# Kernel tuning notes

Measured on AMD Instinct MI355X. Metric: run time of the kernel, lower is better.

Reference implementation:

```python
import jax, jax.numpy as jnp
import numpy as np

B, S, D, H = 2, 2048, 1024, 16
DK = D // H


def setup_inputs() -> dict:
    key = jax.random.key(0)
    ks = jax.random.split(key, 8)
    s = 1.0 / np.sqrt(D)
    return {
        "query": jax.random.normal(ks[0], (B, S, D), jnp.float32),
        "key": jax.random.normal(ks[1], (B, S, D), jnp.float32),
        "value": jax.random.normal(ks[2], (B, S, D), jnp.float32),
        "mask": jnp.ones((B, S), jnp.int32),
        "w_q": jax.random.normal(ks[3], (D, D), jnp.float32) * s,
        "w_k": jax.random.normal(ks[4], (D, D), jnp.float32) * s,
        "w_v": jax.random.normal(ks[5], (D, D), jnp.float32) * s,
        "w_o": jax.random.normal(ks[6], (D, D), jnp.float32) * s,
        "b_o": jnp.zeros((D,), jnp.float32),
    }


def reference(query, key, value, mask, w_q, w_k, w_v, w_o, b_o):
    scale = np.sqrt(DK).astype(np.float32)
    # Linear layers: torch stores weight as [out, in], y = x @ W.T
    Q = (query @ w_q.T).reshape(B, S, H, DK).transpose(0, 2, 1, 3)  # [B,H,S,DK]
    K = (key @ w_k.T).reshape(B, S, H, DK).transpose(0, 2, 1, 3)
    V = (value @ w_v.T).reshape(B, S, H, DK).transpose(0, 2, 1, 3)
    scores = jnp.einsum("bhqd,bhkd->bhqk", Q, K) / scale  # [B,H,S,S]
    m = mask[:, None, None, :]  # [B,1,1,S]
    scores = jnp.where(m == 0, jnp.float32(-1e9), scores)
    attn = jax.nn.softmax(scores, axis=-1)  # dropout in eval mode = identity
    ctx = jnp.einsum("bhqk,bhkd->bhqd", attn, V)
    ctx = ctx.transpose(0, 2, 1, 3).reshape(B, S, D)
    out = ctx @ w_o.T + b_o
    return out, attn
```

## Files before the change

### kernel.cpp

```cpp
#include <hip/hip_runtime.h>
#include <hip/hip_bf16.h>
#include <math.h>

#define B 2
#define S 2048
#define D 1024
#define H 16
#define DK 64

typedef __attribute__((ext_vector_type(8))) short bf8;
typedef __attribute__((ext_vector_type(8))) unsigned short u16x8;
typedef __attribute__((ext_vector_type(4))) unsigned short u16x4;
typedef __attribute__((ext_vector_type(4))) float f32x4;
typedef unsigned short ush;

__device__ __forceinline__ float bf2f(ush u) {
    union { unsigned int i; float f; } v; v.i = ((unsigned int)u) << 16; return v.f;
}
__device__ __forceinline__ ush f2bf_rne(float x) {
    __hip_bfloat16 h = __float2bfloat16(x);
    union { __hip_bfloat16 h; ush u; } v; v.h = h; return v.u;
}
__device__ __forceinline__ ush f2bf_trunc(float x) {
    union { float f; unsigned int i; } v; v.f = x; return (ush)(v.i >> 16);
}

__device__ __forceinline__ void gl16(const void* g, void* l) {
    __builtin_amdgcn_global_load_lds(
        (const __attribute__((address_space(1))) void*)g,
        (__attribute__((address_space(3))) void*)l, 16, 0, 0);
}

#define FENCE()    asm volatile("" ::: "memory")
#define WAIT_VM(N) asm volatile("s_waitcnt vmcnt(" #N ")" ::: "memory")
#define BARRAW()   __builtin_amdgcn_s_barrier()

__global__ __launch_bounds__(256) void conv_tri_k(
    const float* __restrict__ A, ush* __restrict__ Ah, ush* __restrict__ Al, int nbA,
    const float* __restrict__ Bsrc, ush* __restrict__ Bh, ush* __restrict__ Bl, int nbB,
    const float* __restrict__ C, ush* __restrict__ Ch)
{
    const int bx = blockIdx.x;
    const float* src; ush* oh; ush* ol; size_t t;
    if (bx < nbA)            { src = A;    oh = Ah; ol = Al;      t = (size_t)bx * 256 + threadIdx.x; }
    else if (bx < nbA + nbB) { src = Bsrc; oh = Bh; ol = Bl;      t = (size_t)(bx - nbA) * 256 + threadIdx.x; }
    else                     { src = C;    oh = Ch; ol = nullptr; t = (size_t)(bx - nbA - nbB) * 256 + threadIdx.x; }

    const float4* s4 = (const float4*)src + t * 2;
    float4 a = s4[0], c = s4[1];
    float v[8] = {a.x, a.y, a.z, a.w, c.x, c.y, c.z, c.w};
    u16x8 hi;
#pragma unroll
    for (int j = 0; j < 8; ++j) hi[j] = f2bf_trunc(v[j]);
    *(u16x8*)&oh[t * 8] = hi;
    if (ol) {
        u16x8 lo;
#pragma unroll
        for (int j = 0; j < 8; ++j) lo[j] = f2bf_rne(v[j] - bf2f(hi[j]));
        *(u16x8*)&ol[t * 8] = lo;
    }
}

template<bool SPLIT, int EPI>
__global__ __launch_bounds__(256) void gemm_bf2(
    const ush* __restrict__ Xh, const ush* __restrict__ Xl,
    const ush* __restrict__ Wh, const ush* __restrict__ Wl,
    const float* __restrict__ bias, void* __restrict__ Y0v, void* __restrict__ Y1v)
{
    const int tid  = threadIdx.x;
    const int lane = tid & 63;
    const int w    = tid >> 6;
    const int wn   = w >> 1, wm = w & 1;
    const int m0   = blockIdx.x * 64;
    const int n0   = blockIdx.y * 128;

    __shared__ __align__(16) ush Xs[2][128 * 64];
    __shared__ __align__(16) ush Ws[2][64 * 64];

    f32x4 acc[4][2];
#pragma unroll
    for (int s = 0; s < 4; ++s)
#pragma unroll
        for (int t = 0; t < 2; ++t) acc[s][t] = (f32x4){0.f, 0.f, 0.f, 0.f};

    const int kg = (lane >> 4) * 8;
    const int rb = lane >> 3;
    const int jd = lane & 7;
    const int kSteps = SPLIT ? 32 : 16;

    auto stage = [&](ush* Xd, ush* Wd, int ks) {
#pragma unroll
        for (int i = 0; i < 4; ++i) {
            int rd = i * 32 + w * 8 + rb;
            int jo = jd ^ (rd & 7);
            const ush* src;
            if (SPLIT)
                src = (jo < 4) ? Xh + (size_t)(n0 + rd) * 1024 + ks * 32 + jo * 8
                               : Xl + (size_t)(n0 + rd) * 1024 + ks * 32 + (jo - 4) * 8;
            else
                src = Xh + (size_t)(n0 + rd) * 1024 + ks * 64 + jo * 8;
            gl16(src, &Xd[(i * 32 + w * 8) * 64]);
        }
#pragma unroll
        for (int i = 0; i < 2; ++i) {
            int rd = i * 32 + w * 8 + rb;
            int jo = jd ^ (rd & 7);
            const ush* src;
            if (SPLIT)
                src = (jo < 4) ? Wh + (size_t)(m0 + rd) * 1024 + ks * 32 + jo * 8
                               : Wl + (size_t)(m0 + rd) * 1024 + ks * 32 + (jo - 4) * 8;
            else
                src = Wh + (size_t)(m0 + rd) * 1024 + ks * 64 + jo * 8;
            gl16(src, &Wd[(i * 32 + w * 8) * 64]);
        }
    };

    auto step = [&](const ush* Xsrc, const ush* Wsrc) {
        bf8 a0[4], a1[4], b0[2], b1[2];
#pragma unroll
        for (int s = 0; s < 4; ++s) {
            int r = wn * 64 + s * 16 + (lane & 15);
            a0[s] = *(const bf8*)&Xsrc[r * 64 + (kg ^ ((r & 7) << 3))];
            a1[s] = *(const bf8*)&Xsrc[r * 64 + ((32 + kg) ^ ((r & 7) << 3))];
        }
#pragma unroll
        for (int t = 0; t < 2; ++t) {
            int r = wm * 32 + t * 16 + (lane & 15);
            b0[t] = *(const bf8*)&Wsrc[r * 64 + (kg ^ ((r & 7) << 3))];
            b1[t] = *(const bf8*)&Wsrc[r * 64 + ((32 + kg) ^ ((r & 7) << 3))];
        }
#pragma unroll
        for (int s = 0; s < 4; ++s)
#pragma unroll
            for (int t = 0; t < 2; ++t) {
                acc[s][t] = __builtin_amdgcn_mfma_f32_16x16x32_bf16(a0[s], b0[t], acc[s][t], 0, 0, 0);
                if (SPLIT) {
                    acc[s][t] = __builtin_amdgcn_mfma_f32_16x16x32_bf16(a0[s], b1[t], acc[s][t], 0, 0, 0);
                    acc[s][t] = __builtin_amdgcn_mfma_f32_16x16x32_bf16(a1[s], b0[t], acc[s][t], 0, 0, 0);
                } else {
                    acc[s][t] = __builtin_amdgcn_mfma_f32_16x16x32_bf16(a1[s], b1[t], acc[s][t], 0, 0, 0);
                }
            }
    };

    stage(Xs[0], Ws[0], 0);
    FENCE();
    WAIT_VM(0); BARRAW(); FENCE();
    for (int k2 = 0; k2 < kSteps / 2; ++k2) {
        stage(Xs[1], Ws[1], 2 * k2 + 1);
        FENCE();
        step(Xs[0], Ws[0]);
        WAIT_VM(0); BARRAW(); FENCE();
        if (2 * k2 + 2 < kSteps) { stage(Xs[0], Ws[0], 2 * k2 + 2); FENCE(); }
        step(Xs[1], Ws[1]);
        WAIT_VM(0); BARRAW(); FENCE();
    }

#pragma unroll
    for (int s = 0; s < 4; ++s)
#pragma unroll
        for (int t = 0; t < 2; ++t) {
            const int nb = n0 + wn * 64 + 16 * s + 4 * (lane >> 4);
            const int m  = m0 + wm * 32 + 16 * t + (lane & 15);
            if (EPI == 1) {
                ush* Yh = (ush*)Y0v;
                ush* Yl = (ush*)Y1v;
#pragma unroll
                for (int r = 0; r < 4; ++r) {
                    float v = acc[s][t][r];
                    ush hi = f2bf_trunc(v);
                    Yh[(size_t)(nb + r) * 1024 + m] = hi;
                    Yl[(size_t)(nb + r) * 1024 + m] = f2bf_rne(v - bf2f(hi));
                }
            } else {
                ush* Vt = (ush*)Y0v;
                u16x4 pk;
#pragma unroll
                for (int r = 0; r < 4; ++r) pk[r] = f2bf_rne(acc[s][t][r]);
                size_t addr = ((size_t)(nb >> 11) * 1024 + m) * 2048 + (nb & 2047);
                *(u16x4*)&Vt[addr] = pk;
            }
        }
}

__global__ __launch_bounds__(256) void gemm_out(
    const ush* __restrict__ Xb, const float* __restrict__ W,
    const float* __restrict__ bias, float* __restrict__ Y)
{
    const int tid  = threadIdx.x;
    const int lane = tid & 63;
    const int w    = tid >> 6;
    const int wn   = w >> 1, wm = w & 1;
    const int m0   = blockIdx.x * 64;
    const int n0   = blockIdx.y * 128;

    __shared__ __align__(16) ush Xs[128 * 64];
    __shared__ __align__(16) ush Ws[64 * 64];

    f32x4 acc[4][2];
#pragma unroll
    for (int s = 0; s < 4; ++s)
#pragma unroll
        for (int t = 0; t < 2; ++t) acc[s][t] = (f32x4){0.f, 0.f, 0.f, 0.f};

    const int kg = (lane >> 4) * 8;

    for (int k0 = 0; k0 < 1024; k0 += 32) {
        __syncthreads();
#pragma unroll
        for (int i = 0; i < 2; ++i) {
            int cid = i * 256 + tid;
            int r = cid >> 2, c = (cid & 3) * 8;
            u16x8 v = *(const u16x8*)&Xb[(size_t)(n0 + r) * 1024 + k0 + c];
            *(u16x8*)&Xs[r * 64 + (c ^ ((r & 7) << 3))] = v;
        }
#pragma unroll
        for (int i = 0; i < 2; ++i) {
            int cid = i * 256 + tid;
            int r = cid >> 3, c = (cid & 7) * 4;
            float4 v = *(const float4*)&W[(size_t)(m0 + r) * 1024 + k0 + c];
            float vv[4] = {v.x, v.y, v.z, v.w};
            u16x4 hi;
#pragma unroll
            for (int j = 0; j < 4; ++j) hi[j] = f2bf_trunc(vv[j]);
            *(u16x4*)&Ws[r * 64 + (c ^ ((r & 7) << 3))] = hi;
        }
        __syncthreads();

        bf8 ah[4], bh[2];
#pragma unroll
        for (int s = 0; s < 4; ++s) {
            int r = wn * 64 + s * 16 + (lane & 15);
            ah[s] = *(const bf8*)&Xs[r * 64 + (kg ^ ((r & 7) << 3))];
        }
#pragma unroll
        for (int t = 0; t < 2; ++t) {
            int r = wm * 32 + t * 16 + (lane & 15);
            bh[t] = *(const bf8*)&Ws[r * 64 + (kg ^ ((r & 7) << 3))];
        }
#pragma unroll
        for (int s = 0; s < 4; ++s)
#pragma unroll
            for (int t = 0; t < 2; ++t)
                acc[s][t] = __builtin_amdgcn_mfma_f32_16x16x32_bf16(ah[s], bh[t], acc[s][t], 0, 0, 0);
    }

#pragma unroll
    for (int s = 0; s < 4; ++s)
#pragma unroll
        for (int t = 0; t < 2; ++t) {
            const int nb = n0 + wn * 64 + 16 * s + 4 * (lane >> 4);
            const int m  = m0 + wm * 32 + 16 * t + (lane & 15);
            const float bb = bias[m];
#pragma unroll
            for (int r = 0; r < 4; ++r)
                Y[(size_t)(nb + r) * 1024 + m] = acc[s][t][r] + bb;
        }
}

__global__ __launch_bounds__(512) void attn_mfma4(
    const ush* __restrict__ Qh, const ush* __restrict__ Ql,
    const ush* __restrict__ Kh, const ush* __restrict__ Kl,
    const ush* __restrict__ Vt, const int* __restrict__ maskg,
    float* __restrict__ attn, ush* __restrict__ ctx)
{
    const int tid  = threadIdx.x;
    const int lane = tid & 63;
    const int w    = tid >> 6;
    const int lid  = blockIdx.x + (blockIdx.y << 4) + (blockIdx.z << 8);
    const int swz  = ((lid & 7) << 6) | (lid >> 3);
    const int qt = swz & 15, h = (swz >> 4) & 15, b = swz >> 8;
    const int q0 = qt * 128;

    __shared__ __align__(16) ush KhsD[3][4096];
    __shared__ __align__(16) ush KlsD[2][4096];
    __shared__ __align__(16) ush VtsD[2][4096];
    __shared__ __align__(16) ush Pus[8][1024];
    __shared__ float biasS[2048];

    const int kg = (lane >> 4) * 8;
    const int q  = lane & 15;
    const int qrow = q0 + w * 16 + q;
    const int rb = lane >> 3;
    const int jd = lane & 7;

    const ush* KhT = Kh + (size_t)(b * S) * 1024 + h * DK;
    const ush* KlT = Kl + (size_t)(b * S) * 1024 + h * DK;
    const ush* VtT = Vt + (size_t)(b * 1024 + h * DK) * 2048;

    {
        const int t4 = tid * 4;
        int4 mv = *(const int4*)&maskg[b * S + t4];
        biasS[t4 + 0] = mv.x ? 0.f : -1e9f;
        biasS[t4 + 1] = mv.y ? 0.f : -1e9f;
        biasS[t4 + 2] = mv.z ? 0.f : -1e9f;
        biasS[t4 + 3] = mv.w ? 0.f : -1e9f;
    }

    bf8 qh[2], ql[2];
    {
        const ush* p1 = Qh + (size_t)(b * S + qrow) * D + h * DK + kg;
        qh[0] = *(const bf8*)p1; qh[1] = *(const bf8*)(p1 + 32);
        const ush* p2 = Ql + (size_t)(b * S + qrow) * D + h * DK + kg;
        ql[0] = *(const bf8*)p2; ql[1] = *(const bf8*)(p2 + 32);
    }

    const int rd = w * 8 + rb;
    const int jo = jd ^ (rd & 7);

    auto stKh = [&](int bufi, int k0) {
        gl16(KhT + (size_t)(k0 + rd) * 1024 + jo * 8, &KhsD[bufi][(w * 8) * 64]);
    };
    auto stKl = [&](int bufi, int k0) {
        gl16(KlT + (size_t)(k0 + rd) * 1024 + jo * 8, &KlsD[bufi][(w * 8) * 64]);
    };
    auto stVt = [&](int bufi, int k0) {
        gl16(VtT + (size_t)rd * 2048 + k0 + jo * 8, &VtsD[bufi][(w * 8) * 64]);
    };

    const float scale = 0.125f;
    float mrow = -1e30f, lrow = 0.f;

    auto computeA = [&](const ush* Khs_, int k0) {
        f32x4 sacc[4];
#pragma unroll
        for (int st = 0; st < 4; ++st) sacc[st] = (f32x4){0.f, 0.f, 0.f, 0.f};
#pragma unroll
        for (int st = 0; st < 4; ++st) {
            int r = st * 16 + q;
#pragma unroll
            for (int dh = 0; dh < 2; ++dh) {
                bf8 kf = *(const bf8*)&Khs_[r * 64 + ((dh * 32 + kg) ^ ((r & 7) << 3))];
                sacc[st] = __builtin_amdgcn_mfma_f32_16x16x32_bf16(kf, qh[dh], sacc[st], 0, 0, 0);
            }
        }
        f32x4 bias_r[4];
#pragma unroll
        for (int st = 0; st < 4; ++st)
            bias_r[st] = *(const f32x4*)&biasS[k0 + st * 16 + (lane >> 4) * 4];
        float tmax = -1e30f;
#pragma unroll
        for (int st = 0; st < 4; ++st)
#pragma unroll
            for (int rr = 0; rr < 4; ++rr)
                tmax = fmaxf(tmax, sacc[st][rr] * scale + bias_r[st][rr]);
        tmax = fmaxf(tmax, __shfl_xor(tmax, 16));
        tmax = fmaxf(tmax, __shfl_xor(tmax, 32));
        const float nm = fmaxf(mrow, tmax);
        float ts = 0.f;
#pragma unroll
        for (int st = 0; st < 4; ++st)
#pragma unroll
            for (int rr = 0; rr < 4; ++rr)
                ts += __expf(sacc[st][rr] * scale + bias_r[st][rr] - nm);
        ts += __shfl_xor(ts, 16);
        ts += __shfl_xor(ts, 32);
        lrow = lrow * __expf(mrow - nm) + ts;
        mrow = nm;
    };

    stKh(0, 0); stKh(1, 64);
    __syncthreads();
    {
        int cur = 0, nxt = 2;
        for (int kt = 0; kt < 32; ++kt) {
            if (kt + 2 < 32) stKh(nxt, (kt + 2) * 64);
            FENCE();
            computeA(&KhsD[cur][0], kt * 64);
            if (kt < 30) { WAIT_VM(1); } else { WAIT_VM(0); }
            BARRAW(); FENCE();
            cur = (cur == 2) ? 0 : cur + 1;
            nxt = (nxt == 2) ? 0 : nxt + 1;
        }
    }
    const float inv_l = 1.f / lrow;

    f32x4 cacc[4];
#pragma unroll
    for (int dt = 0; dt < 4; ++dt) cacc[dt] = (f32x4){0.f, 0.f, 0.f, 0.f};
    float* attn_bh = attn + (size_t)(b * H + h) * S * S;

    auto computeB = [&](int bsel, int k0) {
        const ush* Khs_ = &KhsD[bsel][0];
        const ush* Kls_ = &KlsD[bsel][0];
        const ush* Vts_ = &VtsD[bsel][0];
        f32x4 sacc[4];
#pragma unroll
        for (int st = 0; st < 4; ++st) sacc[st] = (f32x4){0.f, 0.f, 0.f, 0.f};
#pragma unroll
        for (int st = 0; st < 4; ++st) {
            int r = st * 16 + q;
#pragma unroll
            for (int dh = 0; dh < 2; ++dh) {
                bf8 kf = *(const bf8*)&Khs_[r * 64 + ((dh * 32 + kg) ^ ((r & 7) << 3))];
                bf8 lf = *(const bf8*)&Kls_[r * 64 + ((dh * 32 + kg) ^ ((r & 7) << 3))];
                sacc[st] = __builtin_amdgcn_mfma_f32_16x16x32_bf16(kf, qh[dh], sacc[st], 0, 0, 0);
                sacc[st] = __builtin_amdgcn_mfma_f32_16x16x32_bf16(kf, ql[dh], sacc[st], 0, 0, 0);
                sacc[st] = __builtin_amdgcn_mfma_f32_16x16x32_bf16(lf, qh[dh], sacc[st], 0, 0, 0);
            }
        }
#pragma unroll
        for (int st = 0; st < 4; ++st) {
            f32x4 bias_r = *(const f32x4*)&biasS[k0 + st * 16 + (lane >> 4) * 4];
            float pv[4];
#pragma unroll
            for (int rr = 0; rr < 4; ++rr)
                pv[rr] = __expf(sacc[st][rr] * scale + bias_r[rr] - mrow) * inv_l;
            float4 f4 = {pv[0], pv[1], pv[2], pv[3]};
            *(float4*)&attn_bh[(size_t)(q0 + w * 16 + q) * S + k0 + st * 16 + (lane >> 4) * 4] = f4;
#pragma unroll
            for (int rp = 0; rp < 2; ++rp) {
                int key = st * 16 + (lane >> 4) * 4 + rp * 2;
                unsigned int pk = (unsigned int)f2bf_rne(pv[rp * 2]) |
                                  ((unsigned int)f2bf_rne(pv[rp * 2 + 1]) << 16);
                *(unsigned int*)&Pus[w][q * 64 + (key ^ ((q & 7) << 3))] = pk;
            }
        }
        bf8 pa[2];
        pa[0] = *(const bf8*)&Pus[w][q * 64 + ((kg)      ^ ((q & 7) << 3))];
        pa[1] = *(const bf8*)&Pus[w][q * 64 + ((32 + kg) ^ ((q & 7) << 3))];
#pragma unroll
        for (int dt = 0; dt < 4; ++dt) {
            int r = dt * 16 + q;
#pragma unroll
            for (int kc2 = 0; kc2 < 2; ++kc2) {
                bf8 vf = *(const bf8*)&Vts_[r * 64 + ((kc2 * 32 + kg) ^ ((r & 7) << 3))];
                cacc[dt] = __builtin_amdgcn_mfma_f32_16x16x32_bf16(pa[kc2], vf, cacc[dt], 0, 0, 0);
            }
        }
    };

    stKh(0, 0); stKl(0, 0); stVt(0, 0);
    FENCE();
    WAIT_VM(0); BARRAW(); FENCE();
    {
        int cur = 0;
        for (int kt = 0; kt < 32; ++kt) {
            if (kt + 1 < 32) {
                const int kN = (kt + 1) * 64;
                stKh(cur ^ 1, kN); stKl(cur ^ 1, kN); stVt(cur ^ 1, kN);
            }
            FENCE();
            computeB(cur, kt * 64);
            if (kt + 1 < 32) { WAIT_VM(4); } else { FENCE(); }
            BARRAW(); FENCE();
            cur ^= 1;
        }
    }

#pragma unroll
    for (int dt = 0; dt < 4; ++dt)
#pragma unroll
        for (int rr = 0; rr < 4; ++rr) {
            int qq = q0 + w * 16 + 4 * (lane >> 4) + rr;
            ctx[(size_t)(b * S + qq) * D + h * DK + dt * 16 + (lane & 15)] =
                f2bf_rne(cacc[dt][rr]);
        }
}

extern "C" void kernel_launch(void* const* d_in, const int* in_sizes, int n_in,
                              void* d_out, int out_size, void* d_ws, size_t ws_size,
                              hipStream_t stream)
{
    const float* query = (const float*)d_in[0];
    const float* key   = (const float*)d_in[1];
    const float* value = (const float*)d_in[2];
    const int*   mask  = (const int*)d_in[3];
    const float* w_q   = (const float*)d_in[4];
    const float* w_k   = (const float*)d_in[5];
    const float* w_v   = (const float*)d_in[6];
    const float* w_o   = (const float*)d_in[7];
    const float* b_o   = (const float*)d_in[8];

    float* out  = (float*)d_out;
    float* attn = out + (size_t)B * S * D;

    const size_t NE = (size_t)B * S * D;
    const size_t WE = (size_t)D * D;

    ush* Qh = (ush*)d_ws;
    ush* Ql = Qh + NE;
    ush* Kh = Ql + NE;
    ush* Kl = Kh + NE;
    ush* Vt = Kl + NE;
    ush* Cb = Vt + NE;

    ush* Xh = (ush*)attn;
    ush* Xl = Xh + NE;
    ush* Wh = Xl + NE;
    ush* Wl = Wh + WE;

    const dim3 blk(256);
    const dim3 ggrid(D / 64, (B * S) / 128);
    const dim3 agrid(S / 128, H, B);

    const int nbX = (int)(NE / 8 / 256);
    const int nbW = (int)(WE / 8 / 256);

    conv_tri_k<<<dim3(nbX + nbW), blk, 0, stream>>>(
        query, Xh, Xl, nbX, w_q, Wh, Wl, nbW, nullptr, nullptr);
    gemm_bf2<true, 1><<<ggrid, blk, 0, stream>>>(Xh, Xl, Wh, Wl, nullptr, Qh, Ql);

    conv_tri_k<<<dim3(nbX + nbW), blk, 0, stream>>>(
        key, Xh, Xl, nbX, w_k, Wh, Wl, nbW, nullptr, nullptr);
    gemm_bf2<true, 1><<<ggrid, blk, 0, stream>>>(Xh, Xl, Wh, Wl, nullptr, Kh, Kl);

    conv_tri_k<<<dim3(nbX + nbW), blk, 0, stream>>>(
        value, Xh, nullptr, nbX, w_v, Wh, nullptr, nbW, nullptr, nullptr);
    gemm_bf2<false, 2><<<ggrid, blk, 0, stream>>>(Xh, nullptr, Wh, nullptr, nullptr, Vt, nullptr);

    attn_mfma4<<<agrid, dim3(512), 0, stream>>>(Qh, Ql, Kh, Kl, Vt, mask, attn, Cb);

    gemm_out<<<ggrid, blk, 0, stream>>>(Cb, w_o, b_o, out);
}
```

Before: 355.3 us.

## Use 128x128 512-thread GEMM with 4-stage async pipeline and batch conversions

The projection GEMM moves to 128x128 tiles with 8 waves and a 4-buffer, 3-deep prefetch pipeline driven by partial vmcnt waits, replacing the previous double buffer. The output projection reuses this kernel with a bias epilogue instead of the separate synchronous gemm_out. The earlier conversion passes are merged into two launches by giving each input its own workspace region. The aim is more memory/compute overlap and fewer launches and barriers, at the cost of 128KB of LDS per block, which likely caps occupancy at one block per CU.

New measurement: 344.4 us. 3.1% less time.

```diff
diff --git a/kernel.cpp b/kernel.cpp
--- a/kernel.cpp
+++ b/kernel.cpp
@@ -62,7 +62,7 @@
 }
 
 template<bool SPLIT, int EPI>
-__global__ __launch_bounds__(256) void gemm_bf2(
+__global__ __launch_bounds__(512) void gemm_bf3(
     const ush* __restrict__ Xh, const ush* __restrict__ Xl,
     const ush* __restrict__ Wh, const ush* __restrict__ Wl,
     const float* __restrict__ bias, void* __restrict__ Y0v, void* __restrict__ Y1v)
@@ -70,12 +70,12 @@
     const int tid  = threadIdx.x;
     const int lane = tid & 63;
     const int w    = tid >> 6;
-    const int wn   = w >> 1, wm = w & 1;
-    const int m0   = blockIdx.x * 64;
+    const int wn   = w >> 2;
+    const int wm   = w & 3;
+    const int m0   = blockIdx.x * 128;
     const int n0   = blockIdx.y * 128;
 
-    __shared__ __align__(16) ush Xs[2][128 * 64];
-    __shared__ __align__(16) ush Ws[2][64 * 64];
+    __shared__ __align__(16) ush BufS[4][256 * 64];
 
     f32x4 acc[4][2];
 #pragma unroll
@@ -86,48 +86,45 @@
     const int kg = (lane >> 4) * 8;
     const int rb = lane >> 3;
     const int jd = lane & 7;
-    const int kSteps = SPLIT ? 32 : 16;
-
-    auto stage = [&](ush* Xd, ush* Wd, int ks) {
+    const int kS = SPLIT ? 32 : 16;
+
+    auto stage = [&](ush* buf, int ks) {
 #pragma unroll
         for (int i = 0; i < 4; ++i) {
-            int rd = i * 32 + w * 8 + rb;
+            int rd = w * 32 + i * 8 + rb;
             int jo = jd ^ (rd & 7);
             const ush* src;
-            if (SPLIT)
-                src = (jo < 4) ? Xh + (size_t)(n0 + rd) * 1024 + ks * 32 + jo * 8
-                               : Xl + (size_t)(n0 + rd) * 1024 + ks * 32 + (jo - 4) * 8;
-            else
-                src = Xh + (size_t)(n0 + rd) * 1024 + ks * 64 + jo * 8;
-            gl16(src, &Xd[(i * 32 + w * 8) * 64]);
-        }
-#pragma unroll
-        for (int i = 0; i < 2; ++i) {
-            int rd = i * 32 + w * 8 + rb;
-            int jo = jd ^ (rd & 7);
-            const ush* src;
-            if (SPLIT)
-                src = (jo < 4) ? Wh + (size_t)(m0 + rd) * 1024 + ks * 32 + jo * 8
-                               : Wl + (size_t)(m0 + rd) * 1024 + ks * 32 + (jo - 4) * 8;
-            else
-                src = Wh + (size_t)(m0 + rd) * 1024 + ks * 64 + jo * 8;
-            gl16(src, &Wd[(i * 32 + w * 8) * 64]);
-        }
-    };
-
-    auto step = [&](const ush* Xsrc, const ush* Wsrc) {
+            if (rd < 128) {
+                if (SPLIT)
+                    src = (jo < 4) ? Xh + (size_t)(n0 + rd) * 1024 + ks * 32 + jo * 8
+                                   : Xl + (size_t)(n0 + rd) * 1024 + ks * 32 + (jo - 4) * 8;
+                else
+                    src = Xh + (size_t)(n0 + rd) * 1024 + ks * 64 + jo * 8;
+            } else {
+                int rw = rd - 128;
+                if (SPLIT)
+                    src = (jo < 4) ? Wh + (size_t)(m0 + rw) * 1024 + ks * 32 + jo * 8
+                                   : Wl + (size_t)(m0 + rw) * 1024 + ks * 32 + (jo - 4) * 8;
+                else
+                    src = Wh + (size_t)(m0 + rw) * 1024 + ks * 64 + jo * 8;
+            }
+            gl16(src, &buf[(w * 32 + i * 8) * 64]);
+        }
+    };
+
+    auto step = [&](const ush* buf) {
         bf8 a0[4], a1[4], b0[2], b1[2];
 #pragma unroll
         for (int s = 0; s < 4; ++s) {
             int r = wn * 64 + s * 16 + (lane & 15);
-            a0[s] = *(const bf8*)&Xsrc[r * 64 + (kg ^ ((r & 7) << 3))];
-            a1[s] = *(const bf8*)&Xsrc[r * 64 + ((32 + kg) ^ ((r & 7) << 3))];
+            a0[s] = *(const bf8*)&buf[r * 64 + (kg ^ ((r & 7) << 3))];
+            a1[s] = *(const bf8*)&buf[r * 64 + ((32 + kg) ^ ((r & 7) << 3))];
         }
 #pragma unroll
         for (int t = 0; t < 2; ++t) {
             int r = wm * 32 + t * 16 + (lane & 15);
-            b0[t] = *(const bf8*)&Wsrc[r * 64 + (kg ^ ((r & 7) << 3))];
-            b1[t] = *(const bf8*)&Wsrc[r * 64 + ((32 + kg) ^ ((r & 7) << 3))];
+            b0[t] = *(const bf8*)&buf[(128 + r) * 64 + (kg ^ ((r & 7) << 3))];
+            b1[t] = *(const bf8*)&buf[(128 + r) * 64 + ((32 + kg) ^ ((r & 7) << 3))];
         }
 #pragma unroll
         for (int s = 0; s < 4; ++s)
@@ -143,17 +140,20 @@
             }
     };
 
-    stage(Xs[0], Ws[0], 0);
+    stage(&BufS[0][0], 0);
+    stage(&BufS[1][0], 1);
+    stage(&BufS[2][0], 2);
     FENCE();
-    WAIT_VM(0); BARRAW(); FENCE();
-    for (int k2 = 0; k2 < kSteps / 2; ++k2) {
-        stage(Xs[1], Ws[1], 2 * k2 + 1);
-        FENCE();
-        step(Xs[0], Ws[0]);
-        WAIT_VM(0); BARRAW(); FENCE();
-        if (2 * k2 + 2 < kSteps) { stage(Xs[0], Ws[0], 2 * k2 + 2); FENCE(); }
-        step(Xs[1], Ws[1]);
-        WAIT_VM(0); BARRAW(); FENCE();
+    WAIT_VM(8); BARRAW(); FENCE();
+
+    for (int kt = 0; kt < kS; ++kt) {
+        const int pf = kt + 3;
+        if (pf < kS) { stage(&BufS[pf & 3][0], pf); FENCE(); }
+        step(&BufS[kt & 3][0]);
+        if (kt + 3 < kS)      { WAIT_VM(8); }
+        else if (kt + 2 < kS) { WAIT_VM(4); }
+        else if (kt + 1 < kS) { WAIT_VM(0); }
+        BARRAW(); FENCE();
     }
 
 #pragma unroll
@@ -162,7 +162,13 @@
         for (int t = 0; t < 2; ++t) {
             const int nb = n0 + wn * 64 + 16 * s + 4 * (lane >> 4);
             const int m  = m0 + wm * 32 + 16 * t + (lane & 15);
-            if (EPI == 1) {
+            if (EPI == 0) {
+                float* Y = (float*)Y0v;
+                const float bb = bias[m];
+#pragma unroll
+                for (int r = 0; r < 4; ++r)
+                    Y[(size_t)(nb + r) * 1024 + m] = acc[s][t][r] + bb;
+            } else if (EPI == 1) {
                 ush* Yh = (ush*)Y0v;
                 ush* Yl = (ush*)Y1v;
 #pragma unroll
@@ -180,81 +186,6 @@
                 size_t addr = ((size_t)(nb >> 11) * 1024 + m) * 2048 + (nb & 2047);
                 *(u16x4*)&Vt[addr] = pk;
             }
-        }
-}
-
-__global__ __launch_bounds__(256) void gemm_out(
-    const ush* __restrict__ Xb, const float* __restrict__ W,
-    const float* __restrict__ bias, float* __restrict__ Y)
-{
-    const int tid  = threadIdx.x;
-    const int lane = tid & 63;
-    const int w    = tid >> 6;
-    const int wn   = w >> 1, wm = w & 1;
-    const int m0   = blockIdx.x * 64;
-    const int n0   = blockIdx.y * 128;
-
-    __shared__ __align__(16) ush Xs[128 * 64];
-    __shared__ __align__(16) ush Ws[64 * 64];
-
-    f32x4 acc[4][2];
-#pragma unroll
-    for (int s = 0; s < 4; ++s)
-#pragma unroll
-        for (int t = 0; t < 2; ++t) acc[s][t] = (f32x4){0.f, 0.f, 0.f, 0.f};
-
-    const int kg = (lane >> 4) * 8;
-
-    for (int k0 = 0; k0 < 1024; k0 += 32) {
-        __syncthreads();
-#pragma unroll
-        for (int i = 0; i < 2; ++i) {
-            int cid = i * 256 + tid;
-            int r = cid >> 2, c = (cid & 3) * 8;
-            u16x8 v = *(const u16x8*)&Xb[(size_t)(n0 + r) * 1024 + k0 + c];
-            *(u16x8*)&Xs[r * 64 + (c ^ ((r & 7) << 3))] = v;
-        }
-#pragma unroll
-        for (int i = 0; i < 2; ++i) {
-            int cid = i * 256 + tid;
-            int r = cid >> 3, c = (cid & 7) * 4;
-            float4 v = *(const float4*)&W[(size_t)(m0 + r) * 1024 + k0 + c];
-            float vv[4] = {v.x, v.y, v.z, v.w};
-            u16x4 hi;
-#pragma unroll
-            for (int j = 0; j < 4; ++j) hi[j] = f2bf_trunc(vv[j]);
-            *(u16x4*)&Ws[r * 64 + (c ^ ((r & 7) << 3))] = hi;
-        }
-        __syncthreads();
-
-        bf8 ah[4], bh[2];
-#pragma unroll
-        for (int s = 0; s < 4; ++s) {
-            int r = wn * 64 + s * 16 + (lane & 15);
-            ah[s] = *(const bf8*)&Xs[r * 64 + (kg ^ ((r & 7) << 3))];
-        }
-#pragma unroll
-        for (int t = 0; t < 2; ++t) {
-            int r = wm * 32 + t * 16 + (lane & 15);
-            bh[t] = *(const bf8*)&Ws[r * 64 + (kg ^ ((r & 7) << 3))];
-        }
-#pragma unroll
-        for (int s = 0; s < 4; ++s)
-#pragma unroll
-            for (int t = 0; t < 2; ++t)
-                acc[s][t] = __builtin_amdgcn_mfma_f32_16x16x32_bf16(ah[s], bh[t], acc[s][t], 0, 0, 0);
-    }
-
-#pragma unroll
-    for (int s = 0; s < 4; ++s)
-#pragma unroll
-        for (int t = 0; t < 2; ++t) {
-            const int nb = n0 + wn * 64 + 16 * s + 4 * (lane >> 4);
-            const int m  = m0 + wm * 32 + 16 * t + (lane & 15);
-            const float bb = bias[m];
-#pragma unroll
-            for (int r = 0; r < 4; ++r)
-                Y[(size_t)(nb + r) * 1024 + m] = acc[s][t][r] + bb;
         }
 }
 
@@ -485,31 +416,38 @@
     ush* Vt = Kl + NE;
     ush* Cb = Vt + NE;
 
-    ush* Xh = (ush*)attn;
-    ush* Xl = Xh + NE;
-    ush* Wh = Xl + NE;
-    ush* Wl = Wh + WE;
+    ush* qXh = (ush*)attn;
+    ush* qXl = qXh + NE;
+    ush* kXh = qXl + NE;
+    ush* kXl = kXh + NE;
+    ush* vXh = kXl + NE;
+    ush* wqH = vXh + NE;
+    ush* wqL = wqH + WE;
+    ush* wkH = wqL + WE;
+    ush* wkL = wkH + WE;
+    ush* wvH = wkL + WE;
+    ush* woH = Qh;
 
     const dim3 blk(256);
-    const dim3 ggrid(D / 64, (B * S) / 128);
+    const dim3 gblk(512);
+    const dim3 ggrid(D / 128, (B * S) / 128);
     const dim3 agrid(S / 128, H, B);
 
     const int nbX = (int)(NE / 8 / 256);
     const int nbW = (int)(WE / 8 / 256);
 
-    conv_tri_k<<<dim3(nbX + nbW), blk, 0, stream>>>(
-        query, Xh, Xl, nbX, w_q, Wh, Wl, nbW, nullptr, nullptr);
-    gemm_bf2<true, 1><<<ggrid, blk, 0, stream>>>(Xh, Xl, Wh, Wl, nullptr, Qh, Ql);
-
-    conv_tri_k<<<dim3(nbX + nbW), blk, 0, stream>>>(
-        key, Xh, Xl, nbX, w_k, Wh, Wl, nbW, nullptr, nullptr);
-    gemm_bf2<true, 1><<<ggrid, blk, 0, stream>>>(Xh, Xl, Wh, Wl, nullptr, Kh, Kl);
-
-    conv_tri_k<<<dim3(nbX + nbW), blk, 0, stream>>>(
-        value, Xh, nullptr, nbX, w_v, Wh, nullptr, nbW, nullptr, nullptr);
-    gemm_bf2<false, 2><<<ggrid, blk, 0, stream>>>(Xh, nullptr, Wh, nullptr, nullptr, Vt, nullptr);
+    conv_tri_k<<<dim3(nbX + nbW + nbX), blk, 0, stream>>>(
+        query, qXh, qXl, nbX, w_q, wqH, wqL, nbW, value, vXh);
+    conv_tri_k<<<dim3(nbX + nbW + nbW), blk, 0, stream>>>(
+        key, kXh, kXl, nbX, w_k, wkH, wkL, nbW, w_v, wvH);
+
+    gemm_bf3<true, 1><<<ggrid, gblk, 0, stream>>>(qXh, qXl, wqH, wqL, nullptr, Qh, Ql);
+    gemm_bf3<true, 1><<<ggrid, gblk, 0, stream>>>(kXh, kXl, wkH, wkL, nullptr, Kh, Kl);
+    gemm_bf3<false, 2><<<ggrid, gblk, 0, stream>>>(vXh, nullptr, wvH, nullptr, nullptr, Vt, nullptr);
 
     attn_mfma4<<<agrid, dim3(512), 0, stream>>>(Qh, Ql, Kh, Kl, Vt, mask, attn, Cb);
 
-    gemm_out<<<ggrid, blk, 0, stream>>>(Cb, w_o, b_o, out);
-}
+    conv_tri_k<<<dim3(nbW), blk, 0, stream>>>(
+        nullptr, nullptr, nullptr, 0, nullptr, nullptr, nullptr, 0, w_o, woH);
+    gemm_bf3<false, 0><<<ggrid, gblk, 0, stream>>>(Cb, nullptr, woH, nullptr, b_o, out, nullptr);
+}
```
